# Kernel tuning notes

Measured on AMD Instinct MI355X. Metric: run time of the kernel, lower is better.

The kernel has to match this reference:

```python
import jax, jax.numpy as jnp
import numpy as np

TOP_K = 2

def setup_inputs() -> dict:
    key = jax.random.key(0)
    ks = jax.random.split(key, 6)
    B, S, H, F, E = 2, 2048, 1024, 4096, 8
    s = 0.02
    return {
        "hidden_states": jax.random.normal(ks[0], (B, S, H), dtype=jnp.float32),
        "router_w": jax.random.normal(ks[1], (H, E), dtype=jnp.float32) * s,
        "w1": jax.random.normal(ks[2], (E, H, F), dtype=jnp.float32) * s,
        "b1": jax.random.normal(ks[3], (E, F), dtype=jnp.float32) * s,
        "w2": jax.random.normal(ks[4], (E, F, H), dtype=jnp.float32) * s,
        "b2": jax.random.normal(ks[5], (E, H), dtype=jnp.float32) * s,
    }

def reference(hidden_states, router_w, w1, b1, w2, b2):
    B, S, H = hidden_states.shape
    E = w1.shape[0]
    x = hidden_states.reshape(-1, H)                      # [T, H]
    T = x.shape[0]
    # Router: sigmoid scores, top-k selection (top-1 max path is the k=1 special case)
    scores = jax.nn.sigmoid(x @ router_w)                 # [T, E]
    top_probs, top_idx = jax.lax.top_k(scores, TOP_K)     # [T, K]
    # Dense gate matrix: gate[t, e] = sum_k top_probs[t, k] * (top_idx[t, k] == e)
    gate = jnp.zeros((T, E), dtype=x.dtype).at[jnp.arange(T)[:, None], top_idx].add(top_probs)
    # Run every expert over all tokens (dense reference for the masked gather/scatter loop)
    h = jnp.einsum('th,ehf->etf', x, w1) + b1[:, None, :]  # [E, T, F]
    h = jax.nn.gelu(h, approximate=False)
    y = jnp.einsum('etf,efh->eth', h, w2) + b2[:, None, :]  # [E, T, H]
    out = jnp.einsum('te,eth->th', gate, y)                 # weighted combine
    # dropout with resid_pdrop=0.0 (inference) is identity
    return out.reshape(B, S, H)
```

## Files before the change

kernel.cpp:

```cpp
#include <hip/hip_runtime.h>
#include <math.h>

#define T_TOK 4096
#define HDIM  1024
#define FDIM  4096
#define NEXP  8
#define SLOT_CAP 9216
#define MAXTILES 72

typedef __bf16 bf16x8 __attribute__((ext_vector_type(8)));
typedef float  f32x4  __attribute__((ext_vector_type(4)));

__device__ __forceinline__ void gload_lds16(const void* g, void* l) {
  __builtin_amdgcn_global_load_lds((const __attribute__((address_space(1))) void*)g,
                                   (__attribute__((address_space(3))) void*)l,
                                   16, 0, 0);
}

__global__ void router_k(const float* __restrict__ x, const float* __restrict__ rw,
                         __bf16* __restrict__ xb, int* __restrict__ cnt,
                         int* __restrict__ tok_e, int* __restrict__ tok_pos,
                         float* __restrict__ tok_gate) {
  const int wv   = threadIdx.x >> 6;
  const int lane = threadIdx.x & 63;
  const int t = blockIdx.x * 4 + wv;
  const float* xr = x + (size_t)t * HDIM;
  __bf16* xbr = xb + (size_t)t * HDIM;
  float acc[8];
#pragma unroll
  for (int e = 0; e < 8; ++e) acc[e] = 0.0f;
#pragma unroll
  for (int i = 0; i < 16; ++i) {
    int h = lane + (i << 6);
    float xv = xr[h];
    xbr[h] = (__bf16)xv;
    const float4* rp = (const float4*)(rw + h * 8);
    float4 r0 = rp[0], r1 = rp[1];
    acc[0] += xv * r0.x; acc[1] += xv * r0.y; acc[2] += xv * r0.z; acc[3] += xv * r0.w;
    acc[4] += xv * r1.x; acc[5] += xv * r1.y; acc[6] += xv * r1.z; acc[7] += xv * r1.w;
  }
#pragma unroll
  for (int s = 32; s >= 1; s >>= 1) {
#pragma unroll
    for (int e = 0; e < 8; ++e) acc[e] += __shfl_xor(acc[e], s, 64);
  }
  if (lane == 0) {
    float v0 = acc[0]; int b0 = 0;
#pragma unroll
    for (int e = 1; e < 8; ++e) { if (acc[e] > v0) { v0 = acc[e]; b0 = e; } }
    float v1 = -1e30f; int b1i = 0;
#pragma unroll
    for (int e = 0; e < 8; ++e) { if (e != b0 && acc[e] > v1) { v1 = acc[e]; b1i = e; } }
    float g0 = 1.0f / (1.0f + expf(-v0));
    float g1 = 1.0f / (1.0f + expf(-v1));
    int p0 = atomicAdd(&cnt[b0], 1);
    int p1 = atomicAdd(&cnt[b1i], 1);
    tok_e[t * 2] = b0;    tok_e[t * 2 + 1] = b1i;
    tok_pos[t * 2] = p0;  tok_pos[t * 2 + 1] = p1;
    tok_gate[t * 2] = g0; tok_gate[t * 2 + 1] = g1;
  }
}

__global__ void offs_k(const int* __restrict__ cnt, int* __restrict__ offs,
                       int* __restrict__ tile_e, int* __restrict__ tile_m) {
  if (threadIdx.x == 0) {
    int r = 0, t = 0;
    for (int e = 0; e < NEXP; ++e) {
      offs[e] = r;
      int nt = (cnt[e] + 127) >> 7;
      for (int m = 0; m < nt; ++m) { tile_e[t] = e; tile_m[t] = m; ++t; }
      r += nt << 7;
    }
    for (; t < MAXTILES; ++t) { tile_e[t] = 0; tile_m[t] = 1 << 20; }
  }
}

__global__ void build_k(const int* __restrict__ tok_e, const int* __restrict__ tok_pos,
                        const float* __restrict__ tok_gate, const int* __restrict__ offs,
                        int* __restrict__ slot_tok, float* __restrict__ slot_gate) {
  int idx = blockIdx.x * blockDim.x + threadIdx.x;
  int e = tok_e[idx];
  int slot = offs[e] + tok_pos[idx];
  slot_tok[slot] = idx >> 1;
  slot_gate[slot] = tok_gate[idx];
}

__global__ __launch_bounds__(256) void transpose_cvt2(const float* __restrict__ in,
                                                      __bf16* __restrict__ outp,
                                                      int R, int C) {
  __shared__ unsigned int pt[32][68];
  const int e = blockIdx.z;
  const int c0 = blockIdx.x * 32;
  const int r0 = blockIdx.y * 128;
  const int tid = threadIdx.x;
  const float* ibase = in + (size_t)e * R * C + (size_t)r0 * C + c0;
  const int rp = tid >> 3;
  const int cq = (tid & 7) * 4;
#pragma unroll
  for (int i = 0; i < 2; ++i) {
    int p = rp + 32 * i;
    const float4 v0 = *(const float4*)(ibase + (size_t)(2 * p) * C + cq);
    const float4 v1 = *(const float4*)(ibase + (size_t)(2 * p + 1) * C + cq);
    union { __bf16 h[2]; unsigned int u; } pk;
    pk.h[0] = (__bf16)v0.x; pk.h[1] = (__bf16)v1.x; pt[cq + 0][p] = pk.u;
    pk.h[0] = (__bf16)v0.y; pk.h[1] = (__bf16)v1.y; pt[cq + 1][p] = pk.u;
    pk.h[0] = (__bf16)v0.z; pk.h[1] = (__bf16)v1.z; pt[cq + 2][p] = pk.u;
    pk.h[0] = (__bf16)v0.w; pk.h[1] = (__bf16)v1.w; pt[cq + 3][p] = pk.u;
  }
  __syncthreads();
  const int rs = tid & 7;
  const int cc = tid >> 3;
  __bf16* obase = outp + (size_t)e * R * C + (size_t)c0 * R + r0;
#pragma unroll
  for (int i = 0; i < 2; ++i) {
    int ch = rs + 8 * i;
    uint4 v = *(const uint4*)&pt[cc][ch * 4];
    *(uint4*)(obase + (size_t)cc * R + ch * 8) = v;
  }
}

template<bool G1>
__global__ __launch_bounds__(256) void moe_gemm(
    const __bf16* __restrict__ A, const __bf16* __restrict__ B,
    const float* __restrict__ bias,
    __bf16* __restrict__ hout, float* __restrict__ out,
    const int* __restrict__ cnt, const int* __restrict__ offs,
    const int* __restrict__ slot_tok, const float* __restrict__ slot_gate,
    const int* __restrict__ tile_e, const int* __restrict__ tile_m,
    int N, int K)
{
  const int e = tile_e[blockIdx.y];
  const int mtile = tile_m[blockIdx.y];
  const int cnt_e = cnt[e];
  if (mtile * 128 >= cnt_e) return;
  const int offs_e = offs[e];
  const int nbase = blockIdx.x * 128;

  __shared__ __bf16 As[128 * 64];
  __shared__ __bf16 Bs[128 * 64];

  const int tid = threadIdx.x;
  const int w = tid >> 6, lane = tid & 63;
  const int wy = w >> 1, wx = w & 1;
  const int lm = lane & 15, quad = lane >> 4;
  const int lm7 = lane & 7;
  const int srow = lane >> 3;
  const int scol = lane & 7;

  const __bf16* aptr[4];
  const __bf16* bptr[4];
#pragma unroll
  for (int it = 0; it < 4; ++it) {
    int rl = w * 32 + it * 8 + srow;
    long arow;
    if constexpr (G1) {
      int gm = mtile * 128 + rl;
      int tok = (gm < cnt_e) ? slot_tok[offs_e + gm] : 0;
      arow = (long)tok;
    } else {
      arow = (long)(offs_e + mtile * 128 + rl);
    }
    const int swcol = (scol ^ srow) << 3;
    aptr[it] = A + arow * (long)K + swcol;
    bptr[it] = B + ((long)e * N + nbase + rl) * (long)K + swcol;
  }

  f32x4 acc[4][4];
#pragma unroll
  for (int mt = 0; mt < 4; ++mt)
#pragma unroll
    for (int nt = 0; nt < 4; ++nt) acc[mt][nt] = (f32x4){0.f, 0.f, 0.f, 0.f};

  const int ksteps = K >> 6;
  for (int ks = 0; ks < ksteps; ++ks) {
    const int kofs = ks * 64;
#pragma unroll
    for (int it = 0; it < 4; ++it)
      gload_lds16(aptr[it] + kofs, &As[(w * 32 + it * 8) * 64]);
#pragma unroll
    for (int it = 0; it < 4; ++it)
      gload_lds16(bptr[it] + kofs, &Bs[(w * 32 + it * 8) * 64]);
    __syncthreads();

    const bf16x8* Af = reinterpret_cast<const bf16x8*>(As);
    const bf16x8* Bf = reinterpret_cast<const bf16x8*>(Bs);
#pragma unroll
    for (int kf = 0; kf < 2; ++kf) {
      bf16x8 a[4], b[4];
#pragma unroll
      for (int mt = 0; mt < 4; ++mt)
        a[mt] = Af[(wy * 64 + mt * 16 + lm) * 8 + (((kf << 2) + quad) ^ lm7)];
#pragma unroll
      for (int nt = 0; nt < 4; ++nt)
        b[nt] = Bf[(wx * 64 + nt * 16 + lm) * 8 + (((kf << 2) + quad) ^ lm7)];
#pragma unroll
      for (int mt = 0; mt < 4; ++mt)
#pragma unroll
        for (int nt = 0; nt < 4; ++nt)
          acc[mt][nt] = __builtin_amdgcn_mfma_f32_16x16x32_bf16(a[mt], b[nt], acc[mt][nt], 0, 0, 0);
    }
    __syncthreads();
  }

  if constexpr (G1) {
#pragma unroll
    for (int nt = 0; nt < 4; ++nt) {
      int n = nbase + wx * 64 + nt * 16 + lm;
      float bv = bias[e * N + n];
#pragma unroll
      for (int mt = 0; mt < 4; ++mt) {
        int mrow = wy * 64 + mt * 16 + quad * 4;
        f32x4 c = acc[mt][nt];
#pragma unroll
        for (int i = 0; i < 4; ++i) {
          int gm = mtile * 128 + mrow + i;
          if (gm < cnt_e) {
            float v = c[i] + bv;
            v = 0.5f * v * (1.0f + erff(v * 0.70710678118654752f));
            hout[(size_t)(offs_e + gm) * FDIM + n] = (__bf16)v;
          }
        }
      }
    }
  } else {
    float bv[4]; int nn[4];
#pragma unroll
    for (int nt = 0; nt < 4; ++nt) {
      nn[nt] = nbase + wx * 64 + nt * 16 + lm;
      bv[nt] = bias[e * N + nn[nt]];
    }
#pragma unroll
    for (int mt = 0; mt < 4; ++mt) {
      int mrow = wy * 64 + mt * 16 + quad * 4;
#pragma unroll
      for (int i = 0; i < 4; ++i) {
        int gm = mtile * 128 + mrow + i;
        if (gm >= cnt_e) continue;
        int slot = offs_e + gm;
        int t = slot_tok[slot];
        float g = slot_gate[slot];
        float* orow = out + (size_t)t * HDIM;
#pragma unroll
        for (int nt = 0; nt < 4; ++nt) {
          float v = acc[mt][nt][i] + bv[nt];
          atomicAdd(&orow[nn[nt]], g * v);
        }
      }
    }
  }
}

__global__ void ws_too_small_k(float* out, float v) {
  if (threadIdx.x == 0 && blockIdx.x == 0) out[0] = v;
}

extern "C" void kernel_launch(void* const* d_in, const int* in_sizes, int n_in,
                              void* d_out, int out_size, void* d_ws, size_t ws_size,
                              hipStream_t stream) {
  const float* x  = (const float*)d_in[0];
  const float* rw = (const float*)d_in[1];
  const float* w1 = (const float*)d_in[2];
  const float* b1 = (const float*)d_in[3];
  const float* w2 = (const float*)d_in[4];
  const float* b2 = (const float*)d_in[5];
  float* out = (float*)d_out;
  char* ws = (char*)d_ws;

  size_t o = 0;
  size_t o_xb = o;        o += (size_t)T_TOK * HDIM * 2;
  size_t o_w1t = o;       o += (size_t)NEXP * FDIM * HDIM * 2;
  size_t o_w2t = o;       o += (size_t)NEXP * HDIM * FDIM * 2;
  size_t o_hbuf = o;      o += (size_t)SLOT_CAP * FDIM * 2;
  size_t o_slot_tok = o;  o += (size_t)SLOT_CAP * 4;
  size_t o_slot_gate = o; o += (size_t)SLOT_CAP * 4;
  size_t o_tok_e = o;     o += (size_t)T_TOK * 2 * 4;
  size_t o_tok_pos = o;   o += (size_t)T_TOK * 2 * 4;
  size_t o_tok_gate = o;  o += (size_t)T_TOK * 2 * 4;
  size_t o_cnt = o;       o += 64;
  size_t o_offs = o;      o += 64;
  size_t o_tile = o;      o += MAXTILES * 2 * 4;
  const size_t NEED = o;

  hipMemsetAsync(d_out, 0, (size_t)out_size * 4, stream);
  if (ws_size < NEED) {
    ws_too_small_k<<<1, 64, 0, stream>>>(out, (float)ws_size);
    return;
  }

  __bf16* xb   = (__bf16*)(ws + o_xb);
  __bf16* w1t  = (__bf16*)(ws + o_w1t);
  __bf16* w2t  = (__bf16*)(ws + o_w2t);
  __bf16* hbuf = (__bf16*)(ws + o_hbuf);
  int*   slot_tok  = (int*)(ws + o_slot_tok);
  float* slot_gate = (float*)(ws + o_slot_gate);
  int*   tok_e    = (int*)(ws + o_tok_e);
  int*   tok_pos  = (int*)(ws + o_tok_pos);
  float* tok_gate = (float*)(ws + o_tok_gate);
  int*   cnt  = (int*)(ws + o_cnt);
  int*   offs = (int*)(ws + o_offs);
  int*   tile_e = (int*)(ws + o_tile);
  int*   tile_m = tile_e + MAXTILES;

  hipMemsetAsync(cnt, 0, 64, stream);

  transpose_cvt2<<<dim3(FDIM / 32, HDIM / 128, NEXP), 256, 0, stream>>>(w1, w1t, HDIM, FDIM);
  transpose_cvt2<<<dim3(HDIM / 32, FDIM / 128, NEXP), 256, 0, stream>>>(w2, w2t, FDIM, HDIM);

  router_k<<<T_TOK / 4, 256, 0, stream>>>(x, rw, xb, cnt, tok_e, tok_pos, tok_gate);
  offs_k<<<1, 64, 0, stream>>>(cnt, offs, tile_e, tile_m);
  build_k<<<T_TOK * 2 / 256, 256, 0, stream>>>(tok_e, tok_pos, tok_gate, offs, slot_tok, slot_gate);

  moe_gemm<true><<<dim3(FDIM / 128, MAXTILES), 256, 0, stream>>>(
      xb, w1t, b1, hbuf, nullptr, cnt, offs, slot_tok, slot_gate, tile_e, tile_m, FDIM, HDIM);
  moe_gemm<false><<<dim3(HDIM / 128, MAXTILES), 256, 0, stream>>>(
      hbuf, w2t, b2, nullptr, out, cnt, offs, slot_tok, slot_gate, tile_e, tile_m, HDIM, FDIM);
}
```

Baseline: 690.9 us.

## Replace atomic scatter-add with bf16 expert outputs plus gather combine kernel; use tanh GELU

The second GEMM now writes per-slot bf16 outputs to a new buffer instead of issuing float atomicAdds into the output. A new combine kernel then gathers each token's two expert rows and writes the gate-weighted sum directly, which also removes the output memset. The first GEMM's exact erf GELU is replaced by a tanh-style approximation built on exp2 and rcp intrinsics. This trades atomic contention for an extra bf16 round trip, and adds rounding error from both the bf16 intermediate and the approximate GELU.

```diff
diff --git a/kernel.cpp b/kernel.cpp
--- a/kernel.cpp
+++ b/kernel.cpp
@@ -15,6 +15,15 @@
   __builtin_amdgcn_global_load_lds((const __attribute__((address_space(1))) void*)g,
                                    (__attribute__((address_space(3))) void*)l,
                                    16, 0, 0);
+}
+
+__device__ __forceinline__ float gelu_fast(float x) {
+  float x2 = x * x;
+  float p = fmaf(x2, 0.0356774081f, 0.7978845608f);
+  float z = x * p * 2.8853900818f;
+  float e = __builtin_amdgcn_exp2f(z);
+  float r = __builtin_amdgcn_rcpf(e + 1.0f);
+  return fmaf(-x, r, x);
 }
 
 __global__ void router_k(const float* __restrict__ x, const float* __restrict__ rw,
@@ -123,9 +132,9 @@
 __global__ __launch_bounds__(256) void moe_gemm(
     const __bf16* __restrict__ A, const __bf16* __restrict__ B,
     const float* __restrict__ bias,
-    __bf16* __restrict__ hout, float* __restrict__ out,
+    __bf16* __restrict__ hout,
     const int* __restrict__ cnt, const int* __restrict__ offs,
-    const int* __restrict__ slot_tok, const float* __restrict__ slot_gate,
+    const int* __restrict__ slot_tok,
     const int* __restrict__ tile_e, const int* __restrict__ tile_m,
     int N, int K)
 {
@@ -202,52 +211,48 @@
     __syncthreads();
   }
 
-  if constexpr (G1) {
-#pragma unroll
-    for (int nt = 0; nt < 4; ++nt) {
-      int n = nbase + wx * 64 + nt * 16 + lm;
-      float bv = bias[e * N + n];
-#pragma unroll
-      for (int mt = 0; mt < 4; ++mt) {
-        int mrow = wy * 64 + mt * 16 + quad * 4;
-        f32x4 c = acc[mt][nt];
-#pragma unroll
-        for (int i = 0; i < 4; ++i) {
-          int gm = mtile * 128 + mrow + i;
-          if (gm < cnt_e) {
-            float v = c[i] + bv;
-            v = 0.5f * v * (1.0f + erff(v * 0.70710678118654752f));
-            hout[(size_t)(offs_e + gm) * FDIM + n] = (__bf16)v;
-          }
+#pragma unroll
+  for (int nt = 0; nt < 4; ++nt) {
+    int n = nbase + wx * 64 + nt * 16 + lm;
+    float bv = bias[e * N + n];
+#pragma unroll
+    for (int mt = 0; mt < 4; ++mt) {
+      int mrow = wy * 64 + mt * 16 + quad * 4;
+      f32x4 c = acc[mt][nt];
+#pragma unroll
+      for (int i = 0; i < 4; ++i) {
+        int gm = mtile * 128 + mrow + i;
+        if (gm < cnt_e) {
+          float v = c[i] + bv;
+          if constexpr (G1) v = gelu_fast(v);
+          hout[(size_t)(offs_e + gm) * (size_t)N + n] = (__bf16)v;
         }
       }
     }
-  } else {
-    float bv[4]; int nn[4];
-#pragma unroll
-    for (int nt = 0; nt < 4; ++nt) {
-      nn[nt] = nbase + wx * 64 + nt * 16 + lm;
-      bv[nt] = bias[e * N + nn[nt]];
-    }
-#pragma unroll
-    for (int mt = 0; mt < 4; ++mt) {
-      int mrow = wy * 64 + mt * 16 + quad * 4;
-#pragma unroll
-      for (int i = 0; i < 4; ++i) {
-        int gm = mtile * 128 + mrow + i;
-        if (gm >= cnt_e) continue;
-        int slot = offs_e + gm;
-        int t = slot_tok[slot];
-        float g = slot_gate[slot];
-        float* orow = out + (size_t)t * HDIM;
-#pragma unroll
-        for (int nt = 0; nt < 4; ++nt) {
-          float v = acc[mt][nt][i] + bv[nt];
-          atomicAdd(&orow[nn[nt]], g * v);
-        }
-      }
-    }
-  }
+  }
+}
+
+typedef __bf16 bf16x4v __attribute__((ext_vector_type(4)));
+__global__ __launch_bounds__(256) void combine_k(const __bf16* __restrict__ y,
+                                                 const int* __restrict__ tok_e,
+                                                 const int* __restrict__ tok_pos,
+                                                 const float* __restrict__ tok_gate,
+                                                 const int* __restrict__ offs,
+                                                 float* __restrict__ out) {
+  const int t = blockIdx.x;
+  const int e0 = tok_e[t * 2], e1 = tok_e[t * 2 + 1];
+  const long s0 = offs[e0] + tok_pos[t * 2];
+  const long s1 = offs[e1] + tok_pos[t * 2 + 1];
+  const float g0 = tok_gate[t * 2], g1 = tok_gate[t * 2 + 1];
+  const int h0 = threadIdx.x * 4;
+  bf16x4v a = *(const bf16x4v*)(y + s0 * HDIM + h0);
+  bf16x4v b = *(const bf16x4v*)(y + s1 * HDIM + h0);
+  float4 o;
+  o.x = g0 * (float)a[0] + g1 * (float)b[0];
+  o.y = g0 * (float)a[1] + g1 * (float)b[1];
+  o.z = g0 * (float)a[2] + g1 * (float)b[2];
+  o.w = g0 * (float)a[3] + g1 * (float)b[3];
+  *(float4*)(out + (size_t)t * HDIM + h0) = o;
 }
 
 __global__ void ws_too_small_k(float* out, float v) {
@@ -271,6 +276,7 @@
   size_t o_w1t = o;       o += (size_t)NEXP * FDIM * HDIM * 2;
   size_t o_w2t = o;       o += (size_t)NEXP * HDIM * FDIM * 2;
   size_t o_hbuf = o;      o += (size_t)SLOT_CAP * FDIM * 2;
+  size_t o_ybuf = o;      o += (size_t)SLOT_CAP * HDIM * 2;
   size_t o_slot_tok = o;  o += (size_t)SLOT_CAP * 4;
   size_t o_slot_gate = o; o += (size_t)SLOT_CAP * 4;
   size_t o_tok_e = o;     o += (size_t)T_TOK * 2 * 4;
@@ -281,7 +287,6 @@
   size_t o_tile = o;      o += MAXTILES * 2 * 4;
   const size_t NEED = o;
 
-  hipMemsetAsync(d_out, 0, (size_t)out_size * 4, stream);
   if (ws_size < NEED) {
     ws_too_small_k<<<1, 64, 0, stream>>>(out, (float)ws_size);
     return;
@@ -291,6 +296,7 @@
   __bf16* w1t  = (__bf16*)(ws + o_w1t);
   __bf16* w2t  = (__bf16*)(ws + o_w2t);
   __bf16* hbuf = (__bf16*)(ws + o_hbuf);
+  __bf16* ybuf = (__bf16*)(ws + o_ybuf);
   int*   slot_tok  = (int*)(ws + o_slot_tok);
   float* slot_gate = (float*)(ws + o_slot_gate);
   int*   tok_e    = (int*)(ws + o_tok_e);
@@ -311,7 +317,8 @@
   build_k<<<T_TOK * 2 / 256, 256, 0, stream>>>(tok_e, tok_pos, tok_gate, offs, slot_tok, slot_gate);
 
   moe_gemm<true><<<dim3(FDIM / 128, MAXTILES), 256, 0, stream>>>(
-      xb, w1t, b1, hbuf, nullptr, cnt, offs, slot_tok, slot_gate, tile_e, tile_m, FDIM, HDIM);
+      xb, w1t, b1, hbuf, cnt, offs, slot_tok, tile_e, tile_m, FDIM, HDIM);
   moe_gemm<false><<<dim3(HDIM / 128, MAXTILES), 256, 0, stream>>>(
-      hbuf, w2t, b2, nullptr, out, cnt, offs, slot_tok, slot_gate, tile_e, tile_m, HDIM, FDIM);
-}
+      hbuf, w2t, b2, ybuf, cnt, offs, slot_tok, tile_e, tile_m, HDIM, FDIM);
+  combine_k<<<T_TOK, 256, 0, stream>>>(ybuf, tok_e, tok_pos, tok_gate, offs, out);
+}
```

Result: faster. 674.5 us (-2.4%).
